# Kernel optimization log

Measured on AMD Instinct MI355X. Metric: run time of the kernel, lower is better.

Reference implementation:

```python
import jax, jax.numpy as jnp
import numpy as np

OUT_SIZE = 7
SPATIAL_SCALE = 0.125
SAMPLE_NUM = 2
N_ORI = 8


def setup_inputs() -> dict:
    key = jax.random.key(0)
    k1, k2, k3, k4, k5, k6 = jax.random.split(key, 6)
    N, C_TOT, H, W = 2, 256, 128, 128
    K = 1000
    features = jax.random.normal(k1, (N, C_TOT, H, W), dtype=jnp.float32)
    img = W / SPATIAL_SCALE  # 1024 px image for this stride-8 level
    batch_ind = jax.random.randint(k2, (K,), 0, N).astype(jnp.float32)
    cx = jax.random.uniform(k3, (K,), minval=0.0, maxval=img)
    cy = jax.random.uniform(k4, (K,), minval=0.0, maxval=img)
    wh = jax.random.uniform(k5, (K, 2), minval=32.0, maxval=256.0)
    theta = jax.random.uniform(k6, (K,), minval=0.0, maxval=2.0 * np.pi)
    rois = jnp.stack([batch_ind, cx, cy, wh[:, 0], wh[:, 1], theta], axis=1)
    return {"features": features, "rois": rois}


def _bilinear_gather(ft_flat, base, y, x, H, W):
    """ft_flat: [N*H*W, C]; base: [K,1] flat batch offsets; y,x: [K,P] sample coords.
    Matches CUDA bilinear_interpolate: zero outside [-1, H]x[-1, W], clamp-to-edge."""
    valid = (y >= -1.0) & (y <= H) & (x >= -1.0) & (x <= W)
    y = jnp.clip(y, 0.0, float(H - 1))
    x = jnp.clip(x, 0.0, float(W - 1))
    y0 = jnp.minimum(jnp.floor(y).astype(jnp.int32), H - 1)
    x0 = jnp.minimum(jnp.floor(x).astype(jnp.int32), W - 1)
    y1 = jnp.minimum(y0 + 1, H - 1)
    x1 = jnp.minimum(x0 + 1, W - 1)
    ly = y - y0.astype(y.dtype)
    lx = x - x0.astype(x.dtype)
    hy = 1.0 - ly
    hx = 1.0 - lx

    def g(yy, xx):
        return jnp.take(ft_flat, base + yy * W + xx, axis=0)  # [K, P, C]

    val = ((hy * hx)[..., None] * g(y0, x0)
           + (hy * lx)[..., None] * g(y0, x1)
           + (ly * hx)[..., None] * g(y1, x0)
           + (ly * lx)[..., None] * g(y1, x1))
    return jnp.where(valid[..., None], val, 0.0)


def reference(features, rois):
    N, C_TOT, H, W = features.shape
    C = C_TOT // N_ORI
    K = rois.shape[0]
    b = rois[:, 0].astype(jnp.int32)
    cx = rois[:, 1] * SPATIAL_SCALE
    cy = rois[:, 2] * SPATIAL_SCALE
    rw = jnp.maximum(rois[:, 3] * SPATIAL_SCALE, 1.0)  # force malformed rois to 1x1
    rh = jnp.maximum(rois[:, 4] * SPATIAL_SCALE, 1.0)
    th = rois[:, 5]

    bin_h = rh / OUT_SIZE
    bin_w = rw / OUT_SIZE
    # Per-axis sample positions in bin units: ph + (i + 0.5)/SAMPLE_NUM, flattened over (bin, subsample)
    idx = jnp.arange(OUT_SIZE * SAMPLE_NUM, dtype=jnp.float32)
    frac = jnp.floor(idx / SAMPLE_NUM) + ((idx % SAMPLE_NUM) + 0.5) / SAMPLE_NUM
    yy = -rh[:, None] / 2.0 + frac[None, :] * bin_h[:, None]  # [K, out*s]
    xx = -rw[:, None] / 2.0 + frac[None, :] * bin_w[:, None]  # [K, out*s]
    cos = jnp.cos(th)[:, None, None]
    sin = jnp.sin(th)[:, None, None]
    # Rotate sample grid about roi center: [K, out*s (y), out*s (x)]
    x = xx[:, None, :] * cos - yy[:, :, None] * sin + cx[:, None, None]
    y = xx[:, None, :] * sin + yy[:, :, None] * cos + cy[:, None, None]
    P = OUT_SIZE * SAMPLE_NUM
    x = x.reshape(K, P * P)
    y = y.reshape(K, P * P)

    ft = jnp.transpose(features, (0, 2, 3, 1)).reshape(N * H * W, C_TOT)
    vals = _bilinear_gather(ft, (b * (H * W))[:, None], y, x, H, W)  # [K, P*P, C_TOT]
    # Average-pool the sample grid (pooling commutes with the linear orientation mix)
    pooled = vals.reshape(K, OUT_SIZE, SAMPLE_NUM, OUT_SIZE, SAMPLE_NUM, C_TOT).mean(axis=(2, 4))

    # Orientation-channel circular alignment with linear interpolation
    ind_f = th * N_ORI / (2.0 * jnp.pi)
    ind0 = jnp.floor(ind_f)
    l_var = ind_f - ind0          # weight for next orientation channel
    r_var = 1.0 - l_var
    ind0 = jnp.mod(ind0.astype(jnp.int32), N_ORI)
    o = jnp.arange(N_ORI, dtype=jnp.int32)
    ind_rot = jnp.mod(o[None, :] - ind0[:, None], N_ORI)      # [K, nO]
    ind_rot_p = jnp.mod(ind_rot + 1, N_ORI)

    pooled = pooled.reshape(K, OUT_SIZE, OUT_SIZE, C, N_ORI)
    take = lambda i: jnp.take_along_axis(pooled, i[:, None, None, None, :], axis=4)
    out = (r_var[:, None, None, None, None] * take(ind_rot)
           + l_var[:, None, None, None, None] * take(ind_rot_p))
    # [K, out, out, C, nO] -> [K, C*nO, out, out] (c-major, orientation-minor channel layout)
    return jnp.transpose(out, (0, 3, 4, 1, 2)).reshape(K, C * N_ORI, OUT_SIZE, OUT_SIZE)
```

## Files before the change

kernel.cpp:

```cpp
#include <hip/hip_runtime.h>
#include <hip/hip_bf16.h>
#include <hip/hip_fp16.h>
#include <math.h>

constexpr int N_    = 2;
constexpr int C_TOT = 256;
constexpr int H_    = 128;
constexpr int W_    = 128;
constexpr int OUTS  = 7;
constexpr int NBIN  = OUTS * OUTS;
constexpr int NSAMP = NBIN * 4;
constexpr int PCH   = C_TOT * NBIN;
constexpr float SCALE = 0.125f;

typedef float f32x4 __attribute__((ext_vector_type(4)));

__device__ __forceinline__ __half2 u2h2(unsigned u) {
  return *reinterpret_cast<__half2*>(&u);
}
__device__ __forceinline__ unsigned h2u(__half2 h) {
  return *reinterpret_cast<unsigned*>(&h);
}

__global__ __launch_bounds__(256) void transpose_nchw_nhwc_f16(
    const float* __restrict__ in, ushort* __restrict__ out) {
  __shared__ float tile[64][65];
  const int nh = blockIdx.z;
  const int n  = nh >> 7;
  const int h  = nh & 127;
  const int c0 = blockIdx.y * 64;
  const int w0 = blockIdx.x * 64;
  const int tx = threadIdx.x;
  const int ty = threadIdx.y;

  const float* src = in + (((size_t)n * C_TOT + c0) * H_ + h) * W_ + w0;
#pragma unroll
  for (int i = 0; i < 16; ++i) {
    const int c = i * 4 + ty;
    tile[c][tx] = src[(size_t)c * (H_ * W_) + tx];
  }
  __syncthreads();
  ushort* dst = out + (((size_t)n * H_ + h) * W_ + w0) * C_TOT + c0;
#pragma unroll
  for (int i = 0; i < 16; ++i) {
    const int w = i * 4 + ty;
    dst[(size_t)w * C_TOT + tx] = __half_as_ushort(__float2half(tile[tx][w]));
  }
}

__global__ __launch_bounds__(512, 8) void os2_rroialign_v8(
    const uint4* __restrict__ ft, const float* __restrict__ rois,
    float* __restrict__ out) {
  __shared__ uint2 obuf[NBIN][64];
  __shared__ int4  sIdx[NSAMP];
  __shared__ uint4 sWh[NSAMP];

  const int k = blockIdx.x;
  const int t = threadIdx.x;

  const float* roi = rois + (size_t)k * 6;
  const float th = roi[5];

  if (t < NSAMP) {
    const int   b  = (int)roi[0];
    const float cx = roi[1] * SCALE;
    const float cy = roi[2] * SCALE;
    const float rw = fmaxf(roi[3] * SCALE, 1.0f);
    const float rh = fmaxf(roi[4] * SCALE, 1.0f);
    const float binw = rw / (float)OUTS;
    const float binh = rh / (float)OUTS;
    const float cs = cosf(th);
    const float sn = sinf(th);

    const int bin = t >> 2;
    const int sub = t & 3;
    const int ph  = bin / 7;
    const int pw  = bin - ph * 7;
    const float fy = (float)ph + ((float)(sub >> 1) + 0.5f) * 0.5f;
    const float fx = (float)pw + ((float)(sub & 1)  + 0.5f) * 0.5f;
    const float yy = -rh * 0.5f + fy * binh;
    const float xx = -rw * 0.5f + fx * binw;
    float x = xx * cs - yy * sn + cx;
    float y = xx * sn + yy * cs + cy;
    const bool valid = (y >= -1.0f) && (y <= (float)H_) &&
                       (x >= -1.0f) && (x <= (float)W_);
    y = fminf(fmaxf(y, 0.0f), (float)(H_ - 1));
    x = fminf(fmaxf(x, 0.0f), (float)(W_ - 1));
    int y0 = (int)floorf(y); if (y0 > H_ - 1) y0 = H_ - 1;
    int x0 = (int)floorf(x); if (x0 > W_ - 1) x0 = W_ - 1;
    const int y1 = min(y0 + 1, H_ - 1);
    const int x1 = min(x0 + 1, W_ - 1);
    const float ly = y - (float)y0, lx = x - (float)x0;
    const float hy = 1.0f - ly,     hx = 1.0f - lx;
    const float m  = valid ? 0.25f : 0.0f;
    const __half2 wa = __float2half2_rn(hy * hx * m);
    const __half2 wb = __float2half2_rn(hy * lx * m);
    const __half2 wc = __float2half2_rn(ly * hx * m);
    const __half2 wd = __float2half2_rn(ly * lx * m);
    uint4 pw4;
    pw4.x = h2u(wa); pw4.y = h2u(wb); pw4.z = h2u(wc); pw4.w = h2u(wd);
    sWh[t] = pw4;
    const int pb = b * (H_ * W_);
    sIdx[t] = make_int4((pb + y0 * W_ + x0) * (C_TOT / 8),
                        (pb + y0 * W_ + x1) * (C_TOT / 8),
                        (pb + y1 * W_ + x0) * (C_TOT / 8),
                        (pb + y1 * W_ + x1) * (C_TOT / 8));
  }

  const float indf = th * 1.27323954473516268615f;
  const float i0f  = floorf(indf);
  const float lv   = indf - i0f;
  const float rv   = 1.0f - lv;
  const int ind0 = __builtin_amdgcn_readfirstlane(((int)i0f) & 7);

  const int w  = t >> 6;
  const int l  = t & 63;
  const int cl = l & 31;
  const bool hiHalf = (l & 32) != 0;
  const int slot = 2 * cl + (hiHalf ? 1 : 0);

  __syncthreads();

  const __half2 zero = __float2half2_rn(0.0f);

  for (int i = w; i < NBIN; i += 8) {
    __half2 a01 = zero, a23 = zero, a45 = zero, a67 = zero;
#pragma unroll
    for (int s = 0; s < 4; ++s) {
      const int4  id = sIdx[i * 4 + s];
      const uint4 wt = sWh[i * 4 + s];
      const int b1 = hiHalf ? id.y : id.x;
      const int b2 = hiHalf ? id.w : id.z;
      const __half2 w1 = u2h2(hiHalf ? wt.y : wt.x);
      const __half2 w2 = u2h2(hiHalf ? wt.w : wt.z);
      const uint4 u1 = ft[b1 + cl];
      const uint4 u2 = ft[b2 + cl];
      a01 = __hfma2(u2h2(u1.x), w1, a01);
      a23 = __hfma2(u2h2(u1.y), w1, a23);
      a45 = __hfma2(u2h2(u1.z), w1, a45);
      a67 = __hfma2(u2h2(u1.w), w1, a67);
      a01 = __hfma2(u2h2(u2.x), w2, a01);
      a23 = __hfma2(u2h2(u2.y), w2, a23);
      a45 = __hfma2(u2h2(u2.z), w2, a45);
      a67 = __hfma2(u2h2(u2.w), w2, a67);
    }
    a01 = __hadd2(a01, u2h2(__shfl_xor(h2u(a01), 32)));
    a23 = __hadd2(a23, u2h2(__shfl_xor(h2u(a23), 32)));
    a45 = __hadd2(a45, u2h2(__shfl_xor(h2u(a45), 32)));
    a67 = __hadd2(a67, u2h2(__shfl_xor(h2u(a67), 32)));
    float p[8];
    float2 f;
    f = __half22float2(a01); p[0] = f.x; p[1] = f.y;
    f = __half22float2(a23); p[2] = f.x; p[3] = f.y;
    f = __half22float2(a45); p[4] = f.x; p[5] = f.y;
    f = __half22float2(a67); p[6] = f.x; p[7] = f.y;
    float r[8];
#pragma unroll
    for (int j = 0; j < 8; ++j) r[j] = rv * p[j] + lv * p[(j + 1) & 7];
    const unsigned q01 = h2u(__floats2half2_rn(r[0], r[1]));
    const unsigned q23 = h2u(__floats2half2_rn(r[2], r[3]));
    const unsigned q45 = h2u(__floats2half2_rn(r[4], r[5]));
    const unsigned q67 = h2u(__floats2half2_rn(r[6], r[7]));
    uint2 pk;
    pk.x = hiHalf ? q45 : q01;
    pk.y = hiHalf ? q67 : q23;
    obuf[i][slot ^ ((i >> 2) & 15)] = pk;
  }

  __syncthreads();

  const __half* ob = (const __half*)obuf;
  float* outk = out + (size_t)k * PCH;
  for (int j4 = t; j4 < PCH / 4; j4 += 512) {
    const int j = j4 * 4;
    f32x4 v;
#pragma unroll
    for (int e = 0; e < 4; ++e) {
      const int je   = j + e;
      const int cout = je / NBIN;
      const int bb   = je - cout * NBIN;
      const int clds = (cout & ~7) | ((cout - ind0) & 7);
      const int sp   = (clds >> 2) ^ ((bb >> 2) & 15);
      v[e] = __half2float(ob[bb * 256 + sp * 4 + (clds & 3)]);
    }
    __builtin_nontemporal_store(v, (f32x4*)(outk + j));
  }
}

__global__ __launch_bounds__(256) void os2_rroialign_nchw(
    const float* __restrict__ ft, const float* __restrict__ rois,
    float* __restrict__ out) {
  __shared__ __align__(16) float outBuf[PCH];
  __shared__ int4   sIdx[NSAMP];
  __shared__ float4 sW[NSAMP];

  const int k = blockIdx.x;
  const int t = threadIdx.x;

  const float* roi = rois + (size_t)k * 6;
  const float th = roi[5];

  if (t < NSAMP) {
    const int   b  = (int)roi[0];
    const float cx = roi[1] * SCALE;
    const float cy = roi[2] * SCALE;
    const float rw = fmaxf(roi[3] * SCALE, 1.0f);
    const float rh = fmaxf(roi[4] * SCALE, 1.0f);
    const float binw = rw / (float)OUTS;
    const float binh = rh / (float)OUTS;
    const float cs = cosf(th);
    const float sn = sinf(th);
    const int bin = t >> 2;
    const int sub = t & 3;
    const int ph  = bin / 7;
    const int pw  = bin - ph * 7;
    const float fy = (float)ph + ((float)(sub >> 1) + 0.5f) * 0.5f;
    const float fx = (float)pw + ((float)(sub & 1)  + 0.5f) * 0.5f;
    const float yy = -rh * 0.5f + fy * binh;
    const float xx = -rw * 0.5f + fx * binw;
    float x = xx * cs - yy * sn + cx;
    float y = xx * sn + yy * cs + cy;
    const bool valid = (y >= -1.0f) && (y <= (float)H_) &&
                       (x >= -1.0f) && (x <= (float)W_);
    y = fminf(fmaxf(y, 0.0f), (float)(H_ - 1));
    x = fminf(fmaxf(x, 0.0f), (float)(W_ - 1));
    int y0 = (int)floorf(y); if (y0 > H_ - 1) y0 = H_ - 1;
    int x0 = (int)floorf(x); if (x0 > W_ - 1) x0 = W_ - 1;
    const int y1 = min(y0 + 1, H_ - 1);
    const int x1 = min(x0 + 1, W_ - 1);
    const float ly = y - (float)y0, lx = x - (float)x0;
    const float hy = 1.0f - ly,     hx = 1.0f - lx;
    const float m  = valid ? 0.25f : 0.0f;
    sW[t] = make_float4(hy * hx * m, hy * lx * m, ly * hx * m, ly * lx * m);
    const int cb = b * C_TOT * H_ * W_;
    sIdx[t] = make_int4(cb + y0 * W_ + x0, cb + y0 * W_ + x1,
                        cb + y1 * W_ + x0, cb + y1 * W_ + x1);
  }

  const float indf = th * 1.27323954473516268615f;
  const float i0f  = floorf(indf);
  const float lv   = indf - i0f;
  const float rv   = 1.0f - lv;
  const int ind0 = ((int)i0f) & 7;
  const int o    = t & 7;
  const int ir   = (o - ind0) & 7;
  const int irp  = (ir + 1) & 7;
  const int grp  = t & 56;
  const int chanOff = t * (H_ * W_);

  __syncthreads();

  for (int bin = 0; bin < NBIN; ++bin) {
    float acc = 0.0f;
#pragma unroll
    for (int s = 0; s < 4; ++s) {
      const int4   id = sIdx[bin * 4 + s];
      const float4 w  = sW[bin * 4 + s];
      acc = fmaf(w.x, ft[id.x + chanOff], acc);
      acc = fmaf(w.y, ft[id.y + chanOff], acc);
      acc = fmaf(w.z, ft[id.z + chanOff], acc);
      acc = fmaf(w.w, ft[id.w + chanOff], acc);
    }
    const float v1 = __shfl(acc, grp | ir,  64);
    const float v2 = __shfl(acc, grp | irp, 64);
    outBuf[t * NBIN + bin] = rv * v1 + lv * v2;
  }

  __syncthreads();
  const float4* ob4 = (const float4*)outBuf;
  float4* o4 = (float4*)(out + (size_t)k * PCH);
#pragma unroll 4
  for (int j = t; j < PCH / 4; j += 256) o4[j] = ob4[j];
}

extern "C" void kernel_launch(void* const* d_in, const int* in_sizes, int n_in,
                              void* d_out, int out_size, void* d_ws, size_t ws_size,
                              hipStream_t stream) {
  const float* features = (const float*)d_in[0];
  const float* rois     = (const float*)d_in[1];
  float* out            = (float*)d_out;
  const int K = in_sizes[1] / 6;

  const size_t ftBytes = (size_t)N_ * C_TOT * H_ * W_ * sizeof(ushort);
  if (ws_size >= ftBytes) {
    ushort* ftT = (ushort*)d_ws;
    dim3 tb(64, 4);
    dim3 tg(W_ / 64, C_TOT / 64, N_ * H_);
    transpose_nchw_nhwc_f16<<<tg, tb, 0, stream>>>(features, ftT);
    os2_rroialign_v8<<<K, 512, 0, stream>>>((const uint4*)ftT, rois, out);
  } else {
    os2_rroialign_nchw<<<K, 256, 0, stream>>>(features, rois, out);
  }
}
```

Baseline: 43.75 us.

## Sort ROIs by spatial tile and map contiguous groups to each XCD

Adds a single-block bitonic sort that orders ROIs by batch and a coarse 8x8 spatial tile. Block indices are then remapped so that each of the eight XCDs (taken from blockIdx & 7) processes a contiguous run of sorted ROIs. The aim is better L2 reuse of the transposed fp16 feature map, since ROIs that sample nearby pixels land on the same XCD. It costs an extra serial launch with many syncthreads before the main kernel, plus one indirection load per block.

```diff
diff --git a/kernel.cpp b/kernel.cpp
--- a/kernel.cpp
+++ b/kernel.cpp
@@ -48,14 +48,56 @@
   }
 }
 
-__global__ __launch_bounds__(512, 8) void os2_rroialign_v8(
+__global__ __launch_bounds__(1024) void sort_rois(
+    const float* __restrict__ rois, int K, int* __restrict__ perm) {
+  __shared__ unsigned a[1024];
+  const int t = threadIdx.x;
+  unsigned v = 0xFFFFFFFFu;
+  if (t < K) {
+    const float* roi = rois + (size_t)t * 6;
+    const int b  = (int)roi[0];
+    const float cx = roi[1] * SCALE;
+    const float cy = roi[2] * SCALE;
+    int tx = (int)(cx * 0.0625f); tx = tx < 0 ? 0 : (tx > 7 ? 7 : tx);
+    int ty = (int)(cy * 0.0625f); ty = ty < 0 ? 0 : (ty > 7 ? 7 : ty);
+    const unsigned key = ((unsigned)b << 6) | ((unsigned)ty << 3) | (unsigned)tx;
+    v = (key << 10) | (unsigned)t;
+  }
+  a[t] = v;
+  __syncthreads();
+  for (int ksz = 2; ksz <= 1024; ksz <<= 1) {
+    for (int jsz = ksz >> 1; jsz > 0; jsz >>= 1) {
+      const int ixj = t ^ jsz;
+      if (ixj > t) {
+        const bool up = (t & ksz) == 0;
+        const unsigned x = a[t], y = a[ixj];
+        if (up ? (x > y) : (x < y)) { a[t] = y; a[ixj] = x; }
+      }
+      __syncthreads();
+    }
+  }
+  if (t < K) perm[t] = (int)(a[t] & 1023u);
+}
+
+__global__ void identity_perm(int K, int* __restrict__ perm) {
+  const int i = blockIdx.x * 256 + threadIdx.x;
+  if (i < K) perm[i] = i;
+}
+
+__global__ __launch_bounds__(512, 8) void os2_rroialign_v9(
     const uint4* __restrict__ ft, const float* __restrict__ rois,
-    float* __restrict__ out) {
+    const int* __restrict__ perm, int K, float* __restrict__ out) {
   __shared__ uint2 obuf[NBIN][64];
   __shared__ int4  sIdx[NSAMP];
   __shared__ uint4 sWh[NSAMP];
 
-  const int k = blockIdx.x;
+  const int bid = blockIdx.x;
+  const int q = K >> 3, r = K & 7;
+  const int xcd = bid & 7;
+  const int base = xcd < r ? xcd * (q + 1) : r * (q + 1) + (xcd - r) * q;
+  const int j = base + (bid >> 3);
+  const int k = perm[j];
+
   const int t = threadIdx.x;
 
   const float* roi = rois + (size_t)k * 6;
@@ -154,13 +196,13 @@
     f = __half22float2(a23); p[2] = f.x; p[3] = f.y;
     f = __half22float2(a45); p[4] = f.x; p[5] = f.y;
     f = __half22float2(a67); p[6] = f.x; p[7] = f.y;
-    float r[8];
-#pragma unroll
-    for (int j = 0; j < 8; ++j) r[j] = rv * p[j] + lv * p[(j + 1) & 7];
-    const unsigned q01 = h2u(__floats2half2_rn(r[0], r[1]));
-    const unsigned q23 = h2u(__floats2half2_rn(r[2], r[3]));
-    const unsigned q45 = h2u(__floats2half2_rn(r[4], r[5]));
-    const unsigned q67 = h2u(__floats2half2_rn(r[6], r[7]));
+    float r8[8];
+#pragma unroll
+    for (int jj = 0; jj < 8; ++jj) r8[jj] = rv * p[jj] + lv * p[(jj + 1) & 7];
+    const unsigned q01 = h2u(__floats2half2_rn(r8[0], r8[1]));
+    const unsigned q23 = h2u(__floats2half2_rn(r8[2], r8[3]));
+    const unsigned q45 = h2u(__floats2half2_rn(r8[4], r8[5]));
+    const unsigned q67 = h2u(__floats2half2_rn(r8[6], r8[7]));
     uint2 pk;
     pk.x = hiHalf ? q45 : q01;
     pk.y = hiHalf ? q67 : q23;
@@ -172,18 +214,18 @@
   const __half* ob = (const __half*)obuf;
   float* outk = out + (size_t)k * PCH;
   for (int j4 = t; j4 < PCH / 4; j4 += 512) {
-    const int j = j4 * 4;
+    const int jo = j4 * 4;
     f32x4 v;
 #pragma unroll
     for (int e = 0; e < 4; ++e) {
-      const int je   = j + e;
+      const int je   = jo + e;
       const int cout = je / NBIN;
       const int bb   = je - cout * NBIN;
       const int clds = (cout & ~7) | ((cout - ind0) & 7);
       const int sp   = (clds >> 2) ^ ((bb >> 2) & 15);
       v[e] = __half2float(ob[bb * 256 + sp * 4 + (clds & 3)]);
     }
-    __builtin_nontemporal_store(v, (f32x4*)(outk + j));
+    __builtin_nontemporal_store(v, (f32x4*)(outk + jo));
   }
 }
 
@@ -282,12 +324,19 @@
   const int K = in_sizes[1] / 6;
 
   const size_t ftBytes = (size_t)N_ * C_TOT * H_ * W_ * sizeof(ushort);
-  if (ws_size >= ftBytes) {
+  const size_t permBytes = (size_t)((K + 255) & ~255) * sizeof(int);
+  if (ws_size >= ftBytes + permBytes) {
     ushort* ftT = (ushort*)d_ws;
+    int* perm   = (int*)((char*)d_ws + ftBytes);
     dim3 tb(64, 4);
     dim3 tg(W_ / 64, C_TOT / 64, N_ * H_);
     transpose_nchw_nhwc_f16<<<tg, tb, 0, stream>>>(features, ftT);
-    os2_rroialign_v8<<<K, 512, 0, stream>>>((const uint4*)ftT, rois, out);
+    if (K <= 1024) {
+      sort_rois<<<1, 1024, 0, stream>>>(rois, K, perm);
+    } else {
+      identity_perm<<<(K + 255) / 256, 256, 0, stream>>>(K, perm);
+    }
+    os2_rroialign_v9<<<K, 512, 0, stream>>>((const uint4*)ftT, rois, perm, K, out);
   } else {
     os2_rroialign_nchw<<<K, 256, 0, stream>>>(features, rois, out);
   }
```

Result: slower. 48.76 us (+11.5%).
